# Kernel optimization log

Hardware: AMD Instinct MI355X
Metric: run time of the kernel (lower is better)

## Reference

```python
import jax, jax.numpy as jnp
import numpy as np
import math

B, S, D = 4, 2048, 1024      # batch, seq, d_model
E, F_EXP = 16, 512           # n_experts_ffn, d_expert_ffn
N_SHARED, K_FFN = 2, 4       # shared experts, routed top-k
N_ROUTED = E - N_SHARED


def setup_inputs() -> dict:
    key = jax.random.key(0)
    k0, k1, k2, k3, k4 = jax.random.split(key, 5)
    token_stream = jax.random.normal(k0, (B, S, D), jnp.float32)
    selection_input = jax.random.normal(k1, (B, S, D), jnp.float32)
    # init per reset_parameters (std_scale = 1.0)
    keys_w = jax.random.normal(k2, (E, D, F_EXP), jnp.float32) / math.sqrt(D)
    values_w = jax.random.normal(k3, (E, F_EXP, D), jnp.float32) / math.sqrt(E * F_EXP)
    expert_sel = jax.random.normal(k4, (E, D), jnp.float32) / math.sqrt(D)
    bias_ffn = jnp.zeros((E,), jnp.float32)  # load-balancing bias buffer
    return {
        "token_stream": token_stream,
        "selection_input": selection_input,
        "keys_w": keys_w,
        "values_w": values_w,
        "expert_sel": expert_sel,
        "bias_ffn": bias_ffn,
    }


def reference(token_stream, selection_input, keys_w, values_w, expert_sel, bias_ffn):
    # ---- routing: sigmoid affinity over all experts ----
    affinity = jax.nn.sigmoid(jnp.einsum("bsd,ed->bse", selection_input, expert_sel))  # [B,S,E]
    # top-k over routed experts (bias only affects ranking, not gathered affinity)
    _, routed_idx = jax.lax.top_k(affinity[..., :N_ROUTED] + bias_ffn[:N_ROUTED], K_FFN)  # [B,S,k]
    shared_idx = jnp.broadcast_to(
        jnp.arange(N_ROUTED, E, dtype=routed_idx.dtype), routed_idx.shape[:-1] + (N_SHARED,)
    )
    sel = jnp.concatenate([routed_idx, shared_idx], axis=-1)  # [B,S,K], K = k + shared
    aff_sel = jnp.take_along_axis(affinity, sel, axis=-1)     # [B,S,K]

    # ---- expert FFN (cvmm = gather / grouped GEMM / weighted scatter) ----
    # dense per-expert key projection, then gather selected experts
    scores_all = jnp.einsum("bsd,edf->bsef", token_stream, keys_w)        # [B,S,E,f]
    scores = jnp.take_along_axis(scores_all, sel[..., None], axis=2)      # [B,S,K,f]
    scores = jax.nn.silu(scores)

    # combine: out = sum_k aff_k * (scores_k @ values[sel_k])
    onehot = jax.nn.one_hot(sel, E, dtype=scores.dtype)                   # [B,S,K,E]
    dispatch = jnp.einsum("bskf,bske->bsef", scores * aff_sel[..., None], onehot)  # [B,S,E,f]
    out = jnp.einsum("bsef,efd->bsd", dispatch, values_w)                 # [B,S,D]
    return out, sel
```

## Files before the change

kernel.cpp:

```cpp
#include <hip/hip_runtime.h>

typedef short short8 __attribute__((ext_vector_type(8)));
typedef float f32x4 __attribute__((ext_vector_type(4)));
typedef unsigned short u16;

#define TOK_N 8192
#define DMODEL 1024
#define NEXP 16
#define FEXP 512
#define NROUTED 14
#define KSEL 6
#define MAXTILES 400

__device__ __forceinline__ u16 f2bf(float f) {
  unsigned u = __float_as_uint(f);
  u += 0x7fff + ((u >> 16) & 1);
  return (u16)(u >> 16);
}

typedef const __attribute__((address_space(1))) unsigned int* gas_p;
typedef __attribute__((address_space(3))) unsigned int* las_p;
__device__ __forceinline__ void gload_lds16(const void* g, void* l) {
  __builtin_amdgcn_global_load_lds((gas_p)g, (las_p)l, 16, 0, 0);
}

__global__ void cast_bf16_k(const float* __restrict__ in, u16* __restrict__ out, int n8) {
  int i = blockIdx.x * blockDim.x + threadIdx.x;
  if (i >= n8) return;
  const float4* p = (const float4*)(in + (size_t)i * 8);
  float4 a = p[0], b = p[1];
  short8 v;
  v[0] = (short)f2bf(a.x); v[1] = (short)f2bf(a.y); v[2] = (short)f2bf(a.z); v[3] = (short)f2bf(a.w);
  v[4] = (short)f2bf(b.x); v[5] = (short)f2bf(b.y); v[6] = (short)f2bf(b.z); v[7] = (short)f2bf(b.w);
  *(short8*)(out + (size_t)i * 8) = v;
}

__global__ void transpose_cast_k(const float* __restrict__ in, u16* __restrict__ out, int R, int C) {
  __shared__ u16 tile[32][33];
  int e = blockIdx.z;
  int c0 = blockIdx.x * 32, r0 = blockIdx.y * 32;
  int x = threadIdx.x, y = threadIdx.y;
  const float* ip = in + ((size_t)e * R + r0) * C + c0;
  #pragma unroll
  for (int i = 0; i < 4; i++)
    tile[y + 8 * i][x] = f2bf(ip[(size_t)(y + 8 * i) * C + x]);
  __syncthreads();
  u16* op = out + ((size_t)e * C + c0) * R + r0;
  #pragma unroll
  for (int i = 0; i < 4; i++)
    op[(size_t)(y + 8 * i) * R + x] = tile[x][y + 8 * i];
}

__global__ void routing_k(const float* __restrict__ selin, const float* __restrict__ esel,
                          const float* __restrict__ bias, float* __restrict__ out_sel,
                          unsigned* __restrict__ sel_pack, float* __restrict__ aff6) {
  int tok = blockIdx.x;
  int t = threadIdx.x;
  int e = t & 15, chunk = t >> 4;
  const float4* r4 = (const float4*)(selin + (size_t)tok * DMODEL + chunk * 64);
  const float4* w4 = (const float4*)(esel + (size_t)e * DMODEL + chunk * 64);
  float p = 0.f;
  #pragma unroll
  for (int i = 0; i < 16; i++) {
    float4 a = r4[i], b = w4[i];
    p += a.x * b.x + a.y * b.y + a.z * b.z + a.w * b.w;
  }
  __shared__ float part[16][17];
  __shared__ float aff[16];
  __shared__ float lbias[NROUTED];
  if (t < NROUTED) lbias[t] = bias[t];
  part[chunk][e] = p;
  __syncthreads();
  if (t < 16) {
    float s = 0.f;
    #pragma unroll
    for (int c = 0; c < 16; c++) s += part[c][t];
    aff[t] = 1.f / (1.f + expf(-s));
  }
  __syncthreads();
  if (t == 0) {
    unsigned pack = 0;
    unsigned taken = 0;
    #pragma unroll
    for (int k = 0; k < 4; k++) {
      float best = -3.4e38f; int bi = 0;
      for (int q = 0; q < NROUTED; q++) {
        if (taken & (1u << q)) continue;
        float v = aff[q] + lbias[q];
        if (v > best) { best = v; bi = q; }
      }
      taken |= 1u << bi;
      pack |= (unsigned)bi << (4 * k);
      out_sel[(size_t)tok * KSEL + k] = (float)bi;
      aff6[(size_t)tok * KSEL + k] = aff[bi];
    }
    pack |= 14u << 16; pack |= 15u << 20;
    out_sel[(size_t)tok * KSEL + 4] = 14.f;
    out_sel[(size_t)tok * KSEL + 5] = 15.f;
    aff6[(size_t)tok * KSEL + 4] = aff[14];
    aff6[(size_t)tok * KSEL + 5] = aff[15];
    sel_pack[tok] = pack;
  }
}

__global__ void scatter_k(const unsigned* __restrict__ sel_pack, const float* __restrict__ aff6,
                          int* __restrict__ counts, int* __restrict__ tokk,
                          float* __restrict__ affl) {
  __shared__ int lcnt[16], lbase[16], lcur[16];
  int t = threadIdx.x;
  int tok = blockIdx.x * 256 + t;
  if (t < 16) lcnt[t] = 0;
  __syncthreads();
  unsigned pack = sel_pack[tok];
  int eid[KSEL];
  #pragma unroll
  for (int k = 0; k < KSEL; k++) {
    eid[k] = (pack >> (4 * k)) & 15;
    atomicAdd(&lcnt[eid[k]], 1);
  }
  __syncthreads();
  if (t < 16) {
    lbase[t] = atomicAdd(&counts[t * 16], lcnt[t]);
    lcur[t] = 0;
  }
  __syncthreads();
  #pragma unroll
  for (int k = 0; k < KSEL; k++) {
    int e = eid[k];
    int slot = lbase[e] + atomicAdd(&lcur[e], 1);
    tokk[e * TOK_N + slot] = tok * 8 + k;
    affl[e * TOK_N + slot] = aff6[(size_t)tok * KSEL + k];
  }
}

__global__ void tilelist_k(const int* __restrict__ counts, int* __restrict__ tiles,
                           int* __restrict__ ntiles) {
  __shared__ int tc[16], pb[16];
  int t = threadIdx.x;
  if (t < 16) tc[t] = (counts[t * 16] + 127) >> 7;
  __syncthreads();
  if (t == 0) {
    int s = 0;
    for (int e = 0; e < 16; e++) { pb[e] = s; s += tc[e]; }
    *ntiles = s;
  }
  __syncthreads();
  if (t < 16) {
    int b = pb[t], n = tc[t];
    for (int i = 0; i < n; i++) tiles[b + i] = t | (i << 8);
  }
}

template<int AK, int PASS>
__global__ __launch_bounds__(256, 4) void moe_gemm_k(
    const u16* __restrict__ Abase, const u16* __restrict__ Bbase,
    const int* __restrict__ counts, const int* __restrict__ tokk,
    const float* __restrict__ affl, const int* __restrict__ tiles,
    const int* __restrict__ ntiles, u16* __restrict__ scores_out,
    float* __restrict__ out) {
  int slot = blockIdx.y;
  if (slot >= *ntiles) return;
  int desc = tiles[slot];
  int e = desc & 15;
  int m0 = (desc >> 8) << 7;
  int cnt = counts[e * 16];
  int n0 = blockIdx.x * 128;
  int t = threadIdx.x;
  int lane = t & 63, w = t >> 6;
  int wr = w >> 1, wc = w & 1;

  __shared__ u16 Al[128][64];
  __shared__ u16 Bl[128][64];

  const int* tl = tokk + e * TOK_N + m0;
  const float* al = affl + e * TOK_N + m0;
  const u16* Bp = Bbase + (size_t)e * 524288;

  f32x4 acc[4][4];
  #pragma unroll
  for (int m = 0; m < 4; m++)
    #pragma unroll
    for (int n = 0; n < 4; n++)
      acc[m][n] = (f32x4){0.f, 0.f, 0.f, 0.f};

  int jj = lane & 7, rl = lane >> 3;
  const u16* ag[4]; const u16* bg[4];
  #pragma unroll
  for (int r = 0; r < 4; r++) {
    int row = r * 32 + w * 8 + rl;
    int lr = (m0 + row < cnt) ? row : 0;
    int tk = tl[lr];
    int ar = (PASS == 2) ? (tk >> 3) : ((tk >> 3) * 6 + (tk & 7));
    int cs = (jj ^ (row & 7)) * 8;
    ag[r] = Abase + (size_t)ar * AK + cs;
    bg[r] = Bp + (size_t)(n0 + row) * AK + cs;
  }

  for (int k0 = 0; k0 < AK; k0 += 64) {
    #pragma unroll
    for (int r = 0; r < 4; r++) {
      gload_lds16(ag[r] + k0, &Al[r * 32 + w * 8][0]);
      gload_lds16(bg[r] + k0, &Bl[r * 32 + w * 8][0]);
    }
    __syncthreads();
    #pragma unroll
    for (int kk = 0; kk < 2; kk++) {
      int lc = kk * 4 + (lane >> 4);
      short8 af[4], bf[4];
      #pragma unroll
      for (int m = 0; m < 4; m++) {
        int row = wr * 64 + m * 16 + (lane & 15);
        af[m] = *(const short8*)&Al[row][(lc ^ (row & 7)) * 8];
      }
      #pragma unroll
      for (int n = 0; n < 4; n++) {
        int row = wc * 64 + n * 16 + (lane & 15);
        bf[n] = *(const short8*)&Bl[row][(lc ^ (row & 7)) * 8];
      }
      #pragma unroll
      for (int m = 0; m < 4; m++)
        #pragma unroll
        for (int n = 0; n < 4; n++)
          acc[m][n] = __builtin_amdgcn_mfma_f32_16x16x32_bf16(af[m], bf[n], acc[m][n], 0, 0, 0);
    }
    __syncthreads();
  }

  int cbase = n0 + wc * 64 + (lane & 15);
  #pragma unroll
  for (int m = 0; m < 4; m++) {
    int rbase = wr * 64 + m * 16 + ((lane >> 4) << 2);
    #pragma unroll
    for (int q = 0; q < 4; q++) {
      int row = rbase + q;
      if (m0 + row >= cnt) continue;
      int tk = tl[row];
      if (PASS == 2) {
        float aff = al[row];
        size_t base = (size_t)((tk >> 3) * 6 + (tk & 7)) * FEXP;
        #pragma unroll
        for (int n = 0; n < 4; n++) {
          float v = acc[m][n][q];
          float s = aff * v / (1.f + expf(-v));
          scores_out[base + cbase + n * 16] = f2bf(s);
        }
      } else {
        size_t base = (size_t)(tk >> 3) * DMODEL;
        #pragma unroll
        for (int n = 0; n < 4; n++)
          atomicAdd(&out[base + cbase + n * 16], acc[m][n][q]);
      }
    }
  }
}

extern "C" void kernel_launch(void* const* d_in, const int* in_sizes, int n_in,
                              void* d_out, int out_size, void* d_ws, size_t ws_size,
                              hipStream_t stream) {
  (void)in_sizes; (void)n_in; (void)out_size; (void)ws_size;
  const float* token_stream    = (const float*)d_in[0];
  const float* selection_input = (const float*)d_in[1];
  const float* keys_w          = (const float*)d_in[2];
  const float* values_w        = (const float*)d_in[3];
  const float* expert_sel      = (const float*)d_in[4];
  const float* bias_ffn        = (const float*)d_in[5];

  float* out     = (float*)d_out;
  float* out_sel = out + (size_t)TOK_N * DMODEL;

  char* ws = (char*)d_ws;
  u16*      Xbf      = (u16*)(ws + 0);
  u16*      keysT    = (u16*)(ws + 16777216);
  u16*      valuesT  = (u16*)(ws + 33554432);
  u16*      scoresbf = (u16*)(ws + 50331648);
  int*      counts   = (int*)(ws + 100663296);
  int*      tokk     = (int*)(ws + 100664320);
  float*    affl     = (float*)(ws + 101188608);
  unsigned* sel_pack = (unsigned*)(ws + 101712896);
  float*    aff6     = (float*)(ws + 101745664);
  int*      tiles    = (int*)(ws + 101942272);
  int*      ntiles   = (int*)(ws + 101946368);

  hipMemsetAsync(out, 0, (size_t)TOK_N * DMODEL * sizeof(float), stream);
  hipMemsetAsync(counts, 0, 1024, stream);

  cast_bf16_k<<<4096, 256, 0, stream>>>(token_stream, Xbf, TOK_N * DMODEL / 8);
  transpose_cast_k<<<dim3(16, 32, 16), dim3(32, 8), 0, stream>>>(keys_w, keysT, 1024, 512);
  transpose_cast_k<<<dim3(32, 16, 16), dim3(32, 8), 0, stream>>>(values_w, valuesT, 512, 1024);

  routing_k<<<TOK_N, 256, 0, stream>>>(selection_input, expert_sel, bias_ffn,
                                       out_sel, sel_pack, aff6);
  scatter_k<<<TOK_N / 256, 256, 0, stream>>>(sel_pack, aff6, counts, tokk, affl);
  tilelist_k<<<1, 64, 0, stream>>>(counts, tiles, ntiles);

  moe_gemm_k<1024, 2><<<dim3(4, MAXTILES), 256, 0, stream>>>(Xbf, keysT, counts, tokk, affl,
                                                             tiles, ntiles, scoresbf, nullptr);
  moe_gemm_k<512, 3><<<dim3(8, MAXTILES), 256, 0, stream>>>(scoresbf, valuesT, counts, tokk, affl,
                                                            tiles, ntiles, nullptr, out);
}
```

Measured before the change: 463.5 us.

## Remap MoE GEMM blocks per XCD and store scores contiguously per expert

The 2D grid becomes a 1D grid. Each XCD gets a contiguous range of tile slots, and all N-blocks of a tile run on the same XCD, so the gathered A rows and expert weights stay in that XCD's L2. Intermediate scores are now written in expert-sorted order, using per-expert prefix offsets computed in tilelist_k. That lets the second GEMM read its A rows contiguously instead of through the token index. Launch bounds rise from 4 to 5 blocks per CU, which adds register pressure. The fixed split of slots across XCDs may also leave some XCDs idle when the tile count is low.

```diff
diff --git a/kernel.cpp b/kernel.cpp
--- a/kernel.cpp
+++ b/kernel.cpp
@@ -134,7 +134,7 @@
 }
 
 __global__ void tilelist_k(const int* __restrict__ counts, int* __restrict__ tiles,
-                           int* __restrict__ ntiles) {
+                           int* __restrict__ ntiles, int* __restrict__ pbase) {
   __shared__ int tc[16], pb[16];
   int t = threadIdx.x;
   if (t < 16) tc[t] = (counts[t * 16] + 127) >> 7;
@@ -143,6 +143,8 @@
     int s = 0;
     for (int e = 0; e < 16; e++) { pb[e] = s; s += tc[e]; }
     *ntiles = s;
+    int s2 = 0;
+    for (int e = 0; e < 16; e++) { pbase[e] = s2; s2 += counts[e * 16]; }
   }
   __syncthreads();
   if (t < 16) {
@@ -151,20 +153,25 @@
   }
 }
 
-template<int AK, int PASS>
-__global__ __launch_bounds__(256, 4) void moe_gemm_k(
+template<int AK, int PASS, int NY>
+__global__ __launch_bounds__(256, 5) void moe_gemm_k(
     const u16* __restrict__ Abase, const u16* __restrict__ Bbase,
     const int* __restrict__ counts, const int* __restrict__ tokk,
     const float* __restrict__ affl, const int* __restrict__ tiles,
-    const int* __restrict__ ntiles, u16* __restrict__ scores_out,
-    float* __restrict__ out) {
-  int slot = blockIdx.y;
+    const int* __restrict__ ntiles, const int* __restrict__ pbase,
+    u16* __restrict__ scores_out, float* __restrict__ out) {
+  int p = blockIdx.x;
+  int xcd = p & 7;
+  int i = p >> 3;
+  int slot = xcd * (MAXTILES / 8) + i / NY;
+  int y = i % NY;
   if (slot >= *ntiles) return;
   int desc = tiles[slot];
   int e = desc & 15;
   int m0 = (desc >> 8) << 7;
   int cnt = counts[e * 16];
-  int n0 = blockIdx.x * 128;
+  int pbe = pbase[e];
+  int n0 = y * 128;
   int t = threadIdx.x;
   int lane = t & 63, w = t >> 6;
   int wr = w >> 1, wc = w & 1;
@@ -189,8 +196,13 @@
   for (int r = 0; r < 4; r++) {
     int row = r * 32 + w * 8 + rl;
     int lr = (m0 + row < cnt) ? row : 0;
-    int tk = tl[lr];
-    int ar = (PASS == 2) ? (tk >> 3) : ((tk >> 3) * 6 + (tk & 7));
+    int ar;
+    if (PASS == 2) {
+      int tk = tl[lr];
+      ar = tk >> 3;
+    } else {
+      ar = pbe + m0 + lr;
+    }
     int cs = (jj ^ (row & 7)) * 8;
     ag[r] = Abase + (size_t)ar * AK + cs;
     bg[r] = Bp + (size_t)(n0 + row) * AK + cs;
@@ -234,10 +246,9 @@
     for (int q = 0; q < 4; q++) {
       int row = rbase + q;
       if (m0 + row >= cnt) continue;
-      int tk = tl[row];
       if (PASS == 2) {
         float aff = al[row];
-        size_t base = (size_t)((tk >> 3) * 6 + (tk & 7)) * FEXP;
+        size_t base = (size_t)(pbe + m0 + row) * FEXP;
         #pragma unroll
         for (int n = 0; n < 4; n++) {
           float v = acc[m][n][q];
@@ -245,6 +256,7 @@
           scores_out[base + cbase + n * 16] = f2bf(s);
         }
       } else {
+        int tk = tl[row];
         size_t base = (size_t)(tk >> 3) * DMODEL;
         #pragma unroll
         for (int n = 0; n < 4; n++)
@@ -280,6 +292,7 @@
   float*    aff6     = (float*)(ws + 101745664);
   int*      tiles    = (int*)(ws + 101942272);
   int*      ntiles   = (int*)(ws + 101946368);
+  int*      pbase    = (int*)(ws + 101946432);
 
   hipMemsetAsync(out, 0, (size_t)TOK_N * DMODEL * sizeof(float), stream);
   hipMemsetAsync(counts, 0, 1024, stream);
@@ -291,10 +304,12 @@
   routing_k<<<TOK_N, 256, 0, stream>>>(selection_input, expert_sel, bias_ffn,
                                        out_sel, sel_pack, aff6);
   scatter_k<<<TOK_N / 256, 256, 0, stream>>>(sel_pack, aff6, counts, tokk, affl);
-  tilelist_k<<<1, 64, 0, stream>>>(counts, tiles, ntiles);
-
-  moe_gemm_k<1024, 2><<<dim3(4, MAXTILES), 256, 0, stream>>>(Xbf, keysT, counts, tokk, affl,
-                                                             tiles, ntiles, scoresbf, nullptr);
-  moe_gemm_k<512, 3><<<dim3(8, MAXTILES), 256, 0, stream>>>(scoresbf, valuesT, counts, tokk, affl,
-                                                            tiles, ntiles, nullptr, out);
-}
+  tilelist_k<<<1, 64, 0, stream>>>(counts, tiles, ntiles, pbase);
+
+  moe_gemm_k<1024, 2, 4><<<MAXTILES * 4, 256, 0, stream>>>(Xbf, keysT, counts, tokk, affl,
+                                                           tiles, ntiles, pbase,
+                                                           scoresbf, nullptr);
+  moe_gemm_k<512, 3, 8><<<MAXTILES * 8, 256, 0, stream>>>(scoresbf, valuesT, counts, tokk, affl,
+                                                          tiles, ntiles, pbase,
+                                                          nullptr, out);
+}
```

Measured after the change: 673.4 us. +45.3%, slower.
